# Performance work log

Measured on AMD Instinct MI355X. Metric: run time of the kernel, lower is better.

The kernel has to match this reference:

```python
import math
import jax, jax.numpy as jnp
import numpy as np

# ---- static config (mirrors init_kwargs) ----
NLAT_I, NLON_I = 240, 480      # input equiangular grid (incl. both poles)
NLAT_O, NLON_O = 361, 720      # output equiangular grid (incl. both poles)
CI, CO = 32, 32
NR, NPHI = 3, 3                # kernel_shape
K = (NR - 1) * NPHI + 1        # anisotropic piecewise-linear DISCO basis size = 7
LMAX = 120
CUTOFF = (NR + 0.25) * math.pi / LMAX     # _compute_cutoff_radius
DLAT_O = math.pi / (NLAT_O - 1)
WOFF = int(math.ceil(CUTOFF / DLAT_O))    # half lat-window (=10); geodesic dist >= |dtheta| so window is exact
WLAT = 2 * WOFF + 1
TWO_PI = 2.0 * math.pi


def _bilinear_upsample(x):
    # ResampleS2(mode='bilinear'): x [B,C,NLAT_I,NLON_I] -> [B,C,NLAT_O,NLON_O]
    # equiangular colatitudes theta_j = pi*j/(nlat-1); periodic longitude.
    pos_t = jnp.linspace(0.0, math.pi, NLAT_O) / (math.pi / (NLAT_I - 1))
    i0 = jnp.clip(jnp.floor(pos_t).astype(jnp.int32), 0, NLAT_I - 1)
    i1 = jnp.minimum(i0 + 1, NLAT_I - 1)
    wt = (pos_t - i0).astype(x.dtype)
    xl = (1.0 - wt)[:, None] * x[:, :, i0, :] + wt[:, None] * x[:, :, i1, :]
    pos_p = (jnp.arange(NLON_O) * (TWO_PI / NLON_O)) / (TWO_PI / NLON_I)
    j0f = jnp.floor(pos_p)
    j0 = j0f.astype(jnp.int32) % NLON_I
    j1 = (j0 + 1) % NLON_I
    wp = (pos_p - j0f).astype(x.dtype)
    return (1.0 - wp) * xl[..., j0] + wp * xl[..., j1]


def _build_psi():
    # DISCO filter tensor psi[k, t_out, dlat, dlon] with quadrature merged in,
    # exploiting longitude translation invariance (computed at lon_out = 0).
    theta = jnp.linspace(0.0, math.pi, NLAT_O)
    t_idx = jnp.arange(NLAT_O)
    d_idx = jnp.arange(WLAT) - WOFF
    lat_in = t_idx[:, None] + d_idx[None, :]             # [T,W]
    valid = (lat_in >= 0) & (lat_in < NLAT_O)
    lat_in_c = jnp.clip(lat_in, 0, NLAT_O - 1)
    alpha = -theta[:, None, None]                         # [T,1,1]
    gamma = theta[lat_in_c][:, :, None]                   # [T,W,1]
    beta = (TWO_PI / NLON_O) * jnp.arange(NLON_O)[None, None, :]
    # rotate input point into frame where the output point is at the north pole
    z = jnp.cos(alpha) * jnp.cos(gamma) - jnp.cos(beta) * jnp.sin(alpha) * jnp.sin(gamma)
    xx = jnp.cos(alpha) * jnp.cos(beta) * jnp.sin(gamma) + jnp.sin(alpha) * jnp.cos(gamma)
    yy = jnp.sin(beta) * jnp.sin(gamma)
    r = jnp.arccos(jnp.clip(z, -1.0, 1.0))                # geodesic distance [T,W,P]
    phi = jnp.arctan2(yy, xx) % TWO_PI                    # local azimuth
    dr = CUTOFF / NR
    dph = TWO_PI / NPHI
    vals = [jnp.maximum(0.0, 1.0 - r / dr)]               # isotropic center hat
    for k in range(1, K):
        ir = (k - 1) // NPHI + 1
        ip = (k - 1) % NPHI
        rad = jnp.maximum(0.0, 1.0 - jnp.abs(r - ir * dr) / dr)
        dd = jnp.abs(phi - ip * dph)
        dd = jnp.minimum(dd, TWO_PI - dd)
        az = jnp.maximum(0.0, 1.0 - dd / dph)
        vals.append(rad * az)
    psi = jnp.stack(vals, 0)                              # [K,T,W,P]
    psi = psi * (r <= CUTOFF) * valid[None, :, :, None]
    # merge quadrature weights of the input grid (sin(theta) dtheta dphi)
    q = jnp.sin(theta) * (math.pi / (NLAT_O - 1)) * (TWO_PI / NLON_O)
    psi = psi * q[lat_in_c][None, :, :, None]
    # nodal L1 normalization per basis function and output node
    scale = jnp.sum(psi, axis=(2, 3), keepdims=True)
    psi = psi / jnp.maximum(scale, 1e-8)
    return psi.astype(jnp.float32), lat_in_c


def _disco_conv(xu, weight, psi, lat_in_c):
    # xu [B,Ci,T,P]; weight [Co,Ci,K]; psi [K,T,W,P]
    h = jnp.einsum('oik,bitp->boktp', weight, xu)         # fold channel mixing first
    Hh = jnp.fft.rfft(h, axis=-1)                         # [B,Co,K,T,F]
    Ph = jnp.conj(jnp.fft.rfft(psi, axis=-1))             # [K,T,W,F]
    yh = jnp.zeros(Hh.shape[:2] + (NLAT_O, Hh.shape[-1]), dtype=Hh.dtype)
    for d in range(WLAT):                                 # small fixed halo loop
        Hd = Hh[:, :, :, lat_in_c[:, d], :]               # [B,Co,K,T,F]
        yh = yh + jnp.einsum('boktf,ktf->botf', Hd, Ph[:, :, d, :])
    return jnp.fft.irfft(yh, n=NLON_O, axis=-1)           # circular correlation over lon


def setup_inputs() -> dict:
    key = jax.random.key(0)
    k1, k2 = jax.random.split(key)
    x = jax.random.normal(k1, (1, CI, NLAT_I, NLON_I), dtype=jnp.float32)
    weight = jax.random.normal(k2, (CO, CI, K), dtype=jnp.float32) * 0.05
    return {'x': x, 'weight': weight}


def reference(x, weight):
    psi, lat_in_c = _build_psi()
    xu = _bilinear_upsample(x.astype(jnp.float32))        # forced fp32 region
    y = _disco_conv(xu, weight.astype(jnp.float32), psi, lat_in_c)
    return y.astype(x.dtype)
```

## Files before the change

kernel.cpp:

```cpp
#include <hip/hip_runtime.h>
#include <hip/hip_bf16.h>
#include <math.h>

#define NLAT_I 240
#define NLON_I 480
#define NLAT_O 361
#define NLON_O 720
#define CI_N 32
#define CO_N 32
#define K_N 7
#define WOFF 10
#define WLAT 21

#define PI_F 3.14159265358979323846f
#define TWOPI_F 6.28318530717958647692f
#define DLAT_V (PI_F / 360.0f)
#define DPHI_V (TWOPI_F / 720.0f)
#define CUTOFF_V (3.25f * PI_F / 120.0f)
#define DR_V (CUTOFF_V / 3.0f)
#define IDR_V (1.0f / DR_V)
#define DPH_V (TWOPI_F / 3.0f)
#define IDPH_V (1.0f / DPH_V)
#define QF_V (DLAT_V * DPHI_V)

#define PAD_T 64
#define CT 64
#define NBLK 256
#define NC45 45
#define NE 7581

typedef __attribute__((ext_vector_type(8))) short short8v;
typedef __attribute__((ext_vector_type(4))) short short4v;
typedef __attribute__((ext_vector_type(16))) float f32x16;

__device__ __forceinline__ unsigned short f2bf(float f) {
  __hip_bfloat16 h = __float2bfloat16(f);
  union { __hip_bfloat16 b; unsigned short s; } u; u.b = h; return u.s;
}

__device__ __forceinline__ void psi_eval(float ct, float st, float cg, float sg,
                                         float q, float bang, float v[7]) {
  float sb, cb;
  sincosf(bang, &sb, &cb);
  float dx = sg * cb - st;
  float dy = sg * sb;
  float dz = cg - ct;
  float c2 = dx * dx + dy * dy + dz * dz;
  float r = 2.0f * asinf(fminf(1.0f, 0.5f * sqrtf(c2)));
  if (r <= CUTOFF_V) {
    float xx = ct * cb * sg - st * cg;
    float yy = sb * sg;
    float phi = atan2f(yy, xx);
    if (phi < 0.0f) phi += TWOPI_F;
    v[0] = fmaxf(0.0f, 1.0f - r * IDR_V) * q;
#pragma unroll
    for (int k = 1; k < 7; ++k) {
      const float irdr = (float)(1 + (k - 1) / 3) * DR_V;
      const float ipph = (float)((k - 1) % 3) * DPH_V;
      float rad = fmaxf(0.0f, 1.0f - fabsf(r - irdr) * IDR_V);
      float dd = fabsf(phi - ipph);
      dd = fminf(dd, TWOPI_F - dd);
      float az = fmaxf(0.0f, 1.0f - dd * IDPH_V);
      v[k] = rad * az * q;
    }
  } else {
#pragma unroll
    for (int k = 0; k < 7; ++k) v[k] = 0.0f;
  }
}

__device__ __forceinline__ int windowB(int t, int d) {
  int tp = t + d - WOFF;
  if (tp < 0 || tp > NLAT_O - 1) return -1;
  float th = (float)t * DLAT_V, ga = (float)tp * DLAT_V;
  float st = sinf(th), ct = cosf(th), sg = sinf(ga), cg = cosf(ga);
  float den = st * sg;
  float num = cosf(CUTOFF_V) - ct * cg;
  if (den < 1e-9f) return (fabsf(th - ga) <= CUTOFF_V) ? 360 : -1;
  if (num >= den) return -1;
  if (num <= -den) return 360;
  int B = (int)ceilf(acosf(num / den) * (1.0f / DPHI_V)) + 1;
  return B > 360 ? 360 : B;
}

__device__ __forceinline__ int nsupOf(int B) { return (B >= 360) ? 720 : 2 * B + 1; }
__device__ __forceinline__ int widthOf(int B) {
  return (B < 0) ? 0 : ((nsupOf(B) + 129) & ~1);
}

__global__ void prep_kernel(const float* __restrict__ w, unsigned short* __restrict__ w2,
                            int* __restrict__ offsF, int* __restrict__ offsT,
                            int* __restrict__ wtab, float* __restrict__ sums,
                            int* __restrict__ counter, int* __restrict__ gB,
                            int* __restrict__ gUc) {
  const int tid = threadIdx.x;
  __shared__ int temp[256];
  if (tid < 8) counter[tid] = 0;
  for (int idx = tid; idx < 361 * 7; idx += 256) sums[idx] = 0.0f;
  for (int idx = tid; idx < 14 * 32 * 16; idx += 256) {
    int kk = idx & 15; int o = (idx >> 4) & 31; int c16 = idx >> 9;
    int ci = c16 * 16 + kk; int i = ci & 31; int k = ci >> 5;
    w2[idx] = f2bf(w[(o * 32 + i) * 7 + k]);
  }
  for (int e = tid; e < NE; e += 256) {
    int t = e / 21, d = e % 21;
    int B = windowB(t, d);
    gB[e] = B;
    offsF[e] = (B >= 0) ? nsupOf(B) * 7 : 0;
    offsT[e] = 14 * widthOf(B);
  }
  __syncthreads();
  for (int t = tid; t < 361; t += 256) {
    int run = 0;
    for (int d = 0; d < WLAT; ++d) {
      gUc[t * 22 + d] = run;
      int B = gB[t * 21 + d];
      int np = (B >= 0) ? ((31 + B) >> 4) + ((B + 15) >> 4) + 1 : 0;
      run += np;
    }
    gUc[t * 22 + 21] = run;
    wtab[t] = run;
  }
  __syncthreads();
#pragma unroll 1
  for (int pass = 0; pass < 2; ++pass) {
    int* a = pass ? offsT : offsF;
    int s = tid * 30, e = s + 30; if (e > NE) e = NE; if (s > NE) s = NE;
    int sum = 0;
    for (int i = s; i < e; ++i) sum += a[i];
    temp[tid] = sum;
    __syncthreads();
    if (tid == 0) {
      int run = 0;
      for (int i = 0; i < 256; ++i) { int v = temp[i]; temp[i] = run; run += v; }
      a[NE] = run;
    }
    __syncthreads();
    int run = temp[tid];
    for (int i = s; i < e; ++i) { int v = a[i]; a[i] = run; run += v; }
    __syncthreads();
  }
}

__global__ void upsample_kernel(const float* __restrict__ x,
                                unsigned short* __restrict__ XT) {
  int idx = blockIdx.x * 256 + threadIdx.x;
  if (idx >= NLAT_O * NC45 * 512) return;
  int kk = idx & 15;
  int i = (idx >> 4) & 31;
  int c = (idx >> 9) % NC45;
  int t = idx / (NC45 * 512);
  int p = c * 16 + kk;

  double post = (double)t * (239.0 / 360.0);
  int i0 = (int)floor(post);
  if (i0 < 0) i0 = 0;
  if (i0 > NLAT_I - 1) i0 = NLAT_I - 1;
  int i1 = i0 + 1; if (i1 > NLAT_I - 1) i1 = NLAT_I - 1;
  float wt = (float)(post - (double)i0);

  double posp = (double)p * (2.0 / 3.0);
  double j0f = floor(posp);
  int j0 = ((int)j0f) % NLON_I;
  int j1 = (j0 + 1) % NLON_I;
  float wp = (float)(posp - j0f);

  const float* xi = x + (size_t)i * (NLAT_I * NLON_I);
  float a = xi[i0 * NLON_I + j0];
  float b = xi[i0 * NLON_I + j1];
  float cc = xi[i1 * NLON_I + j0];
  float d = xi[i1 * NLON_I + j1];
  float l0 = (1.0f - wt) * a + wt * cc;
  float l1 = (1.0f - wt) * b + wt * d;
  XT[idx] = f2bf((1.0f - wp) * l0 + wp * l1);
}

__global__ void psi_raw_kernel(const int* __restrict__ offsF,
                               float* __restrict__ PSIF,
                               float* __restrict__ sums) {
  int t = blockIdx.x, d = blockIdx.y;
  int B = windowB(t, d);
  if (B < 0) return;
  int nsup = nsupOf(B);
  int bLo = (B >= 360) ? -360 : -B;
  int offF = offsF[t * 21 + d];
  int tp = t + d - WOFF;
  float th = (float)t * DLAT_V, ga = (float)tp * DLAT_V;
  float st, ct, sg, cg;
  sincosf(th, &st, &ct);
  sincosf(ga, &sg, &cg);
  float q = sg * QF_V;
  float acc[7];
#pragma unroll
  for (int k = 0; k < 7; ++k) acc[k] = 0.0f;
  for (int ix = threadIdx.x; ix < nsup; ix += 256) {
    float v[7];
    psi_eval(ct, st, cg, sg, q, (float)(bLo + ix) * DPHI_V, v);
#pragma unroll
    for (int k = 0; k < 7; ++k) { PSIF[offF + k * nsup + ix] = v[k]; acc[k] += v[k]; }
  }
#pragma unroll
  for (int k = 0; k < 7; ++k) {
    float a = acc[k];
    for (int off = 32; off > 0; off >>= 1) a += __shfl_down(a, off, 64);
    acc[k] = a;
  }
  __shared__ float red[4][7];
  int wid = threadIdx.x >> 6;
  if ((threadIdx.x & 63) == 0) {
#pragma unroll
    for (int k = 0; k < 7; ++k) red[wid][k] = acc[k];
  }
  __syncthreads();
  if (threadIdx.x == 0) {
#pragma unroll
    for (int k = 0; k < 7; ++k)
      atomicAdd(&sums[t * 7 + k], red[0][k] + red[1][k] + red[2][k] + red[3][k]);
  }
}

__global__ void psi_toep_kernel(const int* __restrict__ offsF,
                                const int* __restrict__ offsT,
                                const float* __restrict__ PSIF,
                                const float* __restrict__ sums,
                                unsigned short* __restrict__ PSIT) {
  int t = blockIdx.x, d = blockIdx.y;
  int B = windowB(t, d);
  if (B < 0) return;
  int nsup = nsupOf(B);
  int width = widthOf(B);
  int offF = offsF[t * 21 + d];
  int offT = offsT[t * 21 + d];
  float rc[7];
#pragma unroll
  for (int k = 0; k < 7; ++k) rc[k] = 1.0f / fmaxf(sums[t * 7 + k], 1e-8f);
  for (int ix = threadIdx.x; ix <= width; ix += 256) {
    int isup = ix - PAD_T;
    unsigned short vv[7];
    if (isup >= 0 && isup < nsup) {
#pragma unroll
      for (int k = 0; k < 7; ++k)
        vv[k] = f2bf(PSIF[offF + k * nsup + isup] * rc[k]);
    } else {
#pragma unroll
      for (int k = 0; k < 7; ++k) vv[k] = 0;
    }
    if (ix < width) {
#pragma unroll
      for (int k = 0; k < 7; ++k) PSIT[offT + (2 * k) * width + ix] = vv[k];
    }
    if (ix >= 1) {
#pragma unroll
      for (int k = 0; k < 7; ++k) PSIT[offT + (2 * k + 1) * width + ix - 1] = vv[k];
    }
  }
}


#define LOADSET(S, CC) {                                                  \
    int v45 = pw16 + (CC);                                                \
    if (v45 < 0) v45 += NC45;                                             \
    if (v45 >= NC45) v45 -= NC45;                                         \
    int v45b = v45 + 2; if (v45b >= NC45) v45b -= NC45;                   \
    A##S##a = *(const short8v*)(XT + (((size_t)tpd * NC45 + v45) << 9) + laneA);  \
    A##S##b = *(const short8v*)(XT + (((size_t)tpd * NC45 + v45b) << 9) + laneA); \
    int jbIdx = (CC) * 16 + lconst - bLo + PAD_T;                         \
    const unsigned short* bp = pbase + jbIdx + ((jbIdx & 1) ? (wdt - 1) : 0); \
    B##S##0 = *(const short8v*)(bp);                                      \
    B##S##1 = *(const short8v*)(bp + ks);                                 \
    B##S##2 = *(const short8v*)(bp + 2 * ks);                             \
    B##S##3 = *(const short8v*)(bp + 3 * ks);                             \
    B##S##4 = *(const short8v*)(bp + 4 * ks);                             \
    B##S##5 = *(const short8v*)(bp + 5 * ks);                             \
    B##S##6 = *(const short8v*)(bp + 6 * ks); }

#define MFMASET(S) {                                                      \
    accA0 = __builtin_amdgcn_mfma_f32_32x32x16_bf16(A##S##a, B##S##0, accA0, 0, 0, 0); \
    accB0 = __builtin_amdgcn_mfma_f32_32x32x16_bf16(A##S##b, B##S##0, accB0, 0, 0, 0); \
    accA1 = __builtin_amdgcn_mfma_f32_32x32x16_bf16(A##S##a, B##S##1, accA1, 0, 0, 0); \
    accB1 = __builtin_amdgcn_mfma_f32_32x32x16_bf16(A##S##b, B##S##1, accB1, 0, 0, 0); \
    accA2 = __builtin_amdgcn_mfma_f32_32x32x16_bf16(A##S##a, B##S##2, accA2, 0, 0, 0); \
    accB2 = __builtin_amdgcn_mfma_f32_32x32x16_bf16(A##S##b, B##S##2, accB2, 0, 0, 0); \
    accA3 = __builtin_amdgcn_mfma_f32_32x32x16_bf16(A##S##a, B##S##3, accA3, 0, 0, 0); \
    accB3 = __builtin_amdgcn_mfma_f32_32x32x16_bf16(A##S##b, B##S##3, accB3, 0, 0, 0); \
    accA4 = __builtin_amdgcn_mfma_f32_32x32x16_bf16(A##S##a, B##S##4, accA4, 0, 0, 0); \
    accB4 = __builtin_amdgcn_mfma_f32_32x32x16_bf16(A##S##b, B##S##4, accB4, 0, 0, 0); \
    accA5 = __builtin_amdgcn_mfma_f32_32x32x16_bf16(A##S##a, B##S##5, accA5, 0, 0, 0); \
    accB5 = __builtin_amdgcn_mfma_f32_32x32x16_bf16(A##S##b, B##S##5, accB5, 0, 0, 0); \
    accA6 = __builtin_amdgcn_mfma_f32_32x32x16_bf16(A##S##a, B##S##6, accA6, 0, 0, 0); \
    accB6 = __builtin_amdgcn_mfma_f32_32x32x16_bf16(A##S##b, B##S##6, accB6, 0, 0, 0); }

#define DUMP2(ACC, KK, HB) {                                              \
    short4v q_;                                                           \
    q_[0]=(short)f2bf(ACC[8*(HB)+0]); q_[1]=(short)f2bf(ACC[8*(HB)+1]);   \
    q_[2]=(short)f2bf(ACC[8*(HB)+2]); q_[3]=(short)f2bf(ACC[8*(HB)+3]);   \
    *(short4v*)(b2 + ((KK) << 9) + b0_) = q_;                             \
    q_[0]=(short)f2bf(ACC[8*(HB)+4]); q_[1]=(short)f2bf(ACC[8*(HB)+5]);   \
    q_[2]=(short)f2bf(ACC[8*(HB)+6]); q_[3]=(short)f2bf(ACC[8*(HB)+7]);   \
    *(short4v*)(b2 + ((KK) << 9) + b0_ + 8) = q_; }

#define GEMM2PT(AC0, AC1, AC2, AC3, AC4, AC5, AC6, PTILE) {               \
    f32x16 Dy;                                                            \
    _Pragma("unroll") for (int z = 0; z < 16; ++z) Dy[z] = 0.0f;          \
    DUMP2(AC0, 0, 0) DUMP2(AC1, 1, 0) DUMP2(AC2, 2, 0) DUMP2(AC3, 3, 0)  \
    DUMP2(AC4, 4, 0) DUMP2(AC5, 5, 0) DUMP2(AC6, 6, 0)                    \
    _Pragma("unroll") for (int k2 = 0; k2 < 7; ++k2) {                    \
      short8v A2 = *(const short8v*)(w2g + (((2 * k2 + 0) * 32 + nn) << 4) + g8); \
      short8v B2f = *(const short8v*)(b2 + (k2 << 9) + (nn << 4) + g8);   \
      Dy = __builtin_amdgcn_mfma_f32_32x32x16_bf16(A2, B2f, Dy, 0, 0, 0); \
    }                                                                     \
    DUMP2(AC0, 0, 1) DUMP2(AC1, 1, 1) DUMP2(AC2, 2, 1) DUMP2(AC3, 3, 1)  \
    DUMP2(AC4, 4, 1) DUMP2(AC5, 5, 1) DUMP2(AC6, 6, 1)                    \
    _Pragma("unroll") for (int k2 = 0; k2 < 7; ++k2) {                    \
      short8v A2 = *(const short8v*)(w2g + (((2 * k2 + 1) * 32 + nn) << 4) + g8); \
      short8v B2f = *(const short8v*)(b2 + (k2 << 9) + (nn << 4) + g8);   \
      Dy = __builtin_amdgcn_mfma_f32_32x32x16_bf16(A2, B2f, Dy, 0, 0, 0); \
    }                                                                     \
    const int p_ = (PTILE) * 32 + nn;                                     \
    if (p_ < NLON_O) {                                                    \
      _Pragma("unroll") for (int rr = 0; rr < 16; ++rr) {                 \
        int o = (rr & 3) + 8 * (rr >> 2) + 4 * g;                         \
        atomicAdd(&y[((size_t)o * NLAT_O + t) * NLON_O + p_], Dy[rr]);    \
      }                                                                   \
    } }

__global__ __launch_bounds__(256, 1) void disco_kernel(
    const unsigned short* __restrict__ XT, const unsigned short* __restrict__ PSIT,
    const unsigned short* __restrict__ w2g, const int* __restrict__ offsT,
    const int* __restrict__ wtab, const int* __restrict__ gB,
    const int* __restrict__ gUc, float* __restrict__ y,
    int* __restrict__ counter) {
  const int tid = threadIdx.x;
  __shared__ __align__(16) unsigned short b2all[4 * 3584];
  __shared__ int Sbuf[362];
  __shared__ int sB[WLAT], sUc[WLAT + 1], sOff[WLAT], sW[WLAT];
  __shared__ int curItem, sSv;

  for (int j = tid; j < 361; j += 256) {
    int t = (j & 1) ? 360 - (j >> 1) : (j >> 1);
    Sbuf[j] = 3 * ((wtab[t] + CT - 1) / CT);
  }
  __syncthreads();
  if (tid == 0) {
    int run = 0;
    for (int j = 0; j < 361; ++j) { int v = Sbuf[j]; Sbuf[j] = run; run += v; }
    Sbuf[361] = run;
    sSv = 0;
  }
  __syncthreads();
  const int NTOT = Sbuf[361];
  const int xcd = blockIdx.x & 7;

  const int lane = tid & 63, wv = tid >> 6, nn = lane & 31, g = lane >> 5;
  const int g8 = g * 8;
  const int laneA = nn * 16 + g8;
  const int lconst = g8 - nn;

  while (true) {
    if (tid == 0) {
      int mm = NTOT;
      int s2 = sSv;
      while (s2 < 8) {
        int cx = (xcd + s2) & 7;
        int b0 = (NTOT * cx) >> 3;
        int b1 = (NTOT * (cx + 1)) >> 3;
        int off = atomicAdd(&counter[cx], 1);
        if (b0 + off < b1) { mm = b0 + off; break; }
        ++s2;
      }
      sSv = s2;
      curItem = mm;
    }
    __syncthreads();
    const int m = curItem;
    if (m >= NTOT) break;

    int lo = 0, hi = 360;
    while (lo < hi) {
      int mid = (lo + hi + 1) >> 1;
      if (Sbuf[mid] <= m) lo = mid; else hi = mid - 1;
    }
    const int j = lo;
    const int r = m - Sbuf[j];
    const int t = (j & 1) ? 360 - (j >> 1) : (j >> 1);
    const int pgpair = r % 3;
    const int part = r / 3;

    if (tid < WLAT) {
      int B = gB[t * 21 + tid];
      sB[tid] = B;
      sOff[tid] = offsT[t * 21 + tid];
      sW[tid] = widthOf(B);
    }
    if (tid < WLAT + 1) sUc[tid] = gUc[t * 22 + tid];
    __syncthreads();

    const int Wt = sUc[WLAT];
    int g0 = part * CT, g1 = g0 + CT;
    if (g1 > Wt) g1 = Wt;

    const int ptileA = pgpair * 8 + 2 * wv;
    const int pw16 = ptileA * 2;

    f32x16 accA0, accA1, accA2, accA3, accA4, accA5, accA6;
    f32x16 accB0, accB1, accB2, accB3, accB4, accB5, accB6;
#pragma unroll
    for (int z = 0; z < 16; ++z) {
      accA0[z]=0; accA1[z]=0; accA2[z]=0; accA3[z]=0; accA4[z]=0; accA5[z]=0; accA6[z]=0;
      accB0[z]=0; accB1[z]=0; accB2[z]=0; accB3[z]=0; accB4[z]=0; accB5[z]=0; accB6[z]=0;
    }

    short8v A0a, A0b, A1a, A1b;
    short8v B00, B01, B02, B03, B04, B05, B06;
    short8v B10, B11, B12, B13, B14, B15, B16;

    int gi = g0;
    int d = 0;
    while (d < WLAT && sUc[d + 1] <= gi) ++d;
    while (gi < g1) {
      const int B = sB[d];
      const int bLo = (B >= 360) ? -360 : -B;
      const int cmin = -((B + 15) >> 4);
      const int tpd = t + d - WOFF;
      const int wdt = sW[d];
      const int ks = 2 * wdt;
      const unsigned short* pbase = PSIT + sOff[d];
      const int rend = sUc[d + 1];
      const int gend = (rend < g1) ? rend : g1;
      const int n = gend - gi;
      int c = cmin + (gi - sUc[d]);

      LOADSET(0, c)
      int it = 0;
      for (; it + 2 <= n; it += 2) {
        LOADSET(1, c + 1)
        MFMASET(0)
        if (it + 2 < n) { LOADSET(0, c + 2) }
        MFMASET(1)
        c += 2;
      }
      if (it < n) { MFMASET(0) }

      gi = gend;
      ++d;
      while (d < WLAT && sUc[d + 1] <= gi) ++d;
    }

    unsigned short* b2 = b2all + wv * 3584;
    const int b0_ = nn * 16 + 4 * g;
    GEMM2PT(accA0, accA1, accA2, accA3, accA4, accA5, accA6, ptileA)
    GEMM2PT(accB0, accB1, accB2, accB3, accB4, accB5, accB6, ptileA + 1)
  }
}

extern "C" void kernel_launch(void* const* d_in, const int* in_sizes, int n_in,
                              void* d_out, int out_size, void* d_ws, size_t ws_size,
                              hipStream_t stream) {
  (void)in_sizes; (void)n_in; (void)out_size; (void)ws_size;
  const float* x = (const float*)d_in[0];
  const float* w = (const float*)d_in[1];
  float* y = (float*)d_out;

  unsigned short* XT = (unsigned short*)d_ws;
  float* PSIF = (float*)(XT + (size_t)NLAT_O * NC45 * 512);
  unsigned short* PSIT = (unsigned short*)(PSIF + 6000000);
  unsigned short* w2 = PSIT + 26000000;
  float* sums = (float*)(w2 + 7168);
  int* offsF = (int*)(sums + NLAT_O * K_N);
  int* offsT = offsF + NE + 1;
  int* wtab = offsT + NE + 1;
  int* counter = wtab + 361;
  int* gB = counter + 8;
  int* gUc = gB + NE;

  hipMemsetAsync(y, 0, (size_t)CO_N * NLAT_O * NLON_O * sizeof(float), stream);

  prep_kernel<<<1, 256, 0, stream>>>(w, w2, offsF, offsT, wtab, sums, counter, gB, gUc);
  int n_up = NLAT_O * NC45 * 512;
  upsample_kernel<<<(n_up + 255) / 256, 256, 0, stream>>>(x, XT);
  psi_raw_kernel<<<dim3(NLAT_O, WLAT), 256, 0, stream>>>(offsF, PSIF, sums);
  psi_toep_kernel<<<dim3(NLAT_O, WLAT), 256, 0, stream>>>(offsF, offsT, PSIF, sums, PSIT);
  disco_kernel<<<NBLK, 256, 0, stream>>>(XT, PSIT, w2, offsT, wtab, gB, gUc, y, counter);
}
```

Measured before the change: 532.0 us.

## Stage A/B operand tiles through LDS ring with async global_load_lds pipeline

Replaces the direct per-lane global vector loads of the X and psi operands with a multi-stage LDS ring buffer filled by global_load_lds DMA. The psi rows are shared across the four waves, with each wave fetching part of them. Per-step indexing is precomputed in lane registers and broadcast with readlane, so the inner loop no longer walks the halo structure. The aim is to hide global memory latency and stop each wave from loading psi redundantly, at the cost of a block barrier every step, extra LDS use and reliance on a hand-tuned vmcnt wait.

```diff
diff --git a/kernel.cpp b/kernel.cpp
--- a/kernel.cpp
+++ b/kernel.cpp
@@ -36,6 +36,13 @@
 __device__ __forceinline__ unsigned short f2bf(float f) {
   __hip_bfloat16 h = __float2bfloat16(f);
   union { __hip_bfloat16 b; unsigned short s; } u; u.b = h; return u.s;
+}
+
+typedef __attribute__((address_space(1))) const unsigned int ga_u32_t;
+typedef __attribute__((address_space(3))) unsigned int ls_u32_t;
+__device__ __forceinline__ void dma16(const unsigned short* g, unsigned short* l) {
+  __builtin_amdgcn_global_load_lds((ga_u32_t*)(const void*)g,
+                                   (ls_u32_t*)(void*)l, 16, 0, 0);
 }
 
 __device__ __forceinline__ void psi_eval(float ct, float st, float cg, float sg,
@@ -257,24 +264,47 @@
 }
 
 
-#define LOADSET(S, CC) {                                                  \
-    int v45 = pw16 + (CC);                                                \
-    if (v45 < 0) v45 += NC45;                                             \
-    if (v45 >= NC45) v45 -= NC45;                                         \
-    int v45b = v45 + 2; if (v45b >= NC45) v45b -= NC45;                   \
-    A##S##a = *(const short8v*)(XT + (((size_t)tpd * NC45 + v45) << 9) + laneA);  \
-    A##S##b = *(const short8v*)(XT + (((size_t)tpd * NC45 + v45b) << 9) + laneA); \
-    int jbIdx = (CC) * 16 + lconst - bLo + PAD_T;                         \
-    const unsigned short* bp = pbase + jbIdx + ((jbIdx & 1) ? (wdt - 1) : 0); \
-    B##S##0 = *(const short8v*)(bp);                                      \
-    B##S##1 = *(const short8v*)(bp + ks);                                 \
-    B##S##2 = *(const short8v*)(bp + 2 * ks);                             \
-    B##S##3 = *(const short8v*)(bp + 3 * ks);                             \
-    B##S##4 = *(const short8v*)(bp + 4 * ks);                             \
-    B##S##5 = *(const short8v*)(bp + 5 * ks);                             \
-    B##S##6 = *(const short8v*)(bp + 6 * ks); }
-
-#define MFMASET(S) {                                                      \
+#define VMW16 asm volatile("s_waitcnt vmcnt(16)" ::: "memory");
+#define BARR  __builtin_amdgcn_s_barrier();
+
+#define STAGEU(IDX) {                                                       \
+    int ix_ = (IDX); if (ix_ > nUm1) ix_ = nUm1;                            \
+    int mx_ = __builtin_amdgcn_readlane(mxL, ix_);                          \
+    int my_ = __builtin_amdgcn_readlane(myL, ix_);                          \
+    int wdt_ = my_ & 4095;                                                  \
+    int dd_ = (my_ >> 12) & 31;                                             \
+    int cc_ = ((my_ >> 17) & 63) - 32;                                      \
+    int sl_ = ix_ & 7;                                                      \
+    int jb_ = mx_ + lconst;                                                 \
+    const unsigned short* bs_ = PSIT + jb_ + ((jb_ & 1) ? (wdt_ - 1) : 0);  \
+    unsigned short* bd_ = Bring + sl_ * 3584;                               \
+    int ks_ = 2 * wdt_;                                                     \
+    dma16(bs_ + r0B * ks_, bd_ + (r0B << 9));                               \
+    dma16(bs_ + r1B * ks_, bd_ + (r1B << 9));                               \
+    int v45_ = pw16 + cc_;                                                  \
+    if (v45_ < 0) v45_ += NC45;                                             \
+    if (v45_ >= NC45) v45_ -= NC45;                                         \
+    int v45b_ = v45_ + 2; if (v45b_ >= NC45) v45b_ -= NC45;                 \
+    int tpd_ = t + dd_ - WOFF;                                              \
+    unsigned short* ad_ = Aring + (((wv << 3) + sl_) << 10);                \
+    dma16(XT + (((size_t)(tpd_ * NC45 + v45_)) << 9) + laneA, ad_);         \
+    dma16(XT + (((size_t)(tpd_ * NC45 + v45b_)) << 9) + laneA, ad_ + 512); }
+
+#define READF(S, IDX) {                                                     \
+    int sl_ = (IDX) & 7;                                                    \
+    const unsigned short* bb_ = Bring + sl_ * 3584 + (lane << 3);           \
+    B##S##0 = *(const short8v*)(bb_);                                       \
+    B##S##1 = *(const short8v*)(bb_ + 512);                                 \
+    B##S##2 = *(const short8v*)(bb_ + 1024);                                \
+    B##S##3 = *(const short8v*)(bb_ + 1536);                                \
+    B##S##4 = *(const short8v*)(bb_ + 2048);                                \
+    B##S##5 = *(const short8v*)(bb_ + 2560);                                \
+    B##S##6 = *(const short8v*)(bb_ + 3072);                                \
+    const unsigned short* aa_ = Aring + (((wv << 3) + sl_) << 10) + (lane << 3); \
+    A##S##a = *(const short8v*)(aa_);                                       \
+    A##S##b = *(const short8v*)(aa_ + 512); }
+
+#define MFMA14(S) {                                                         \
     accA0 = __builtin_amdgcn_mfma_f32_32x32x16_bf16(A##S##a, B##S##0, accA0, 0, 0, 0); \
     accB0 = __builtin_amdgcn_mfma_f32_32x32x16_bf16(A##S##b, B##S##0, accB0, 0, 0, 0); \
     accA1 = __builtin_amdgcn_mfma_f32_32x32x16_bf16(A##S##a, B##S##1, accA1, 0, 0, 0); \
@@ -331,6 +361,8 @@
     const int* __restrict__ gUc, float* __restrict__ y,
     int* __restrict__ counter) {
   const int tid = threadIdx.x;
+  __shared__ __align__(16) unsigned short Bring[8 * 3584];
+  __shared__ __align__(16) unsigned short Aring[32 * 1024];
   __shared__ __align__(16) unsigned short b2all[4 * 3584];
   __shared__ int Sbuf[362];
   __shared__ int sB[WLAT], sUc[WLAT + 1], sOff[WLAT], sW[WLAT];
@@ -355,6 +387,8 @@
   const int g8 = g * 8;
   const int laneA = nn * 16 + g8;
   const int lconst = g8 - nn;
+  const int r0B = (wv < 3) ? 2 * wv : 6;
+  const int r1B = (wv < 3) ? 2 * wv + 1 : 6;
 
   while (true) {
     if (tid == 0) {
@@ -398,9 +432,24 @@
     const int Wt = sUc[WLAT];
     int g0 = part * CT, g1 = g0 + CT;
     if (g1 > Wt) g1 = Wt;
+    const int nU = g1 - g0;
+    const int nUm1 = nU - 1;
 
     const int ptileA = pgpair * 8 + 2 * wv;
     const int pw16 = ptileA * 2;
+
+    int mxL, myL;
+    {
+      int uu_ = lane; if (uu_ > nUm1) uu_ = nUm1;
+      int ug_ = g0 + uu_;
+      int dd = 0;
+      while (dd < 20 && sUc[dd + 1] <= ug_) ++dd;
+      int Bv = sB[dd];
+      int bLo_ = (Bv >= 360) ? -360 : -Bv;
+      int cc_ = -((Bv + 15) >> 4) + (ug_ - sUc[dd]);
+      mxL = sOff[dd] + cc_ * 16 - bLo_ + PAD_T;
+      myL = sW[dd] | (dd << 12) | ((cc_ + 32) << 17);
+    }
 
     f32x16 accA0, accA1, accA2, accA3, accA4, accA5, accA6;
     f32x16 accB0, accB1, accB2, accB3, accB4, accB5, accB6;
@@ -410,40 +459,28 @@
       accB0[z]=0; accB1[z]=0; accB2[z]=0; accB3[z]=0; accB4[z]=0; accB5[z]=0; accB6[z]=0;
     }
 
-    short8v A0a, A0b, A1a, A1b;
-    short8v B00, B01, B02, B03, B04, B05, B06;
-    short8v B10, B11, B12, B13, B14, B15, B16;
-
-    int gi = g0;
-    int d = 0;
-    while (d < WLAT && sUc[d + 1] <= gi) ++d;
-    while (gi < g1) {
-      const int B = sB[d];
-      const int bLo = (B >= 360) ? -360 : -B;
-      const int cmin = -((B + 15) >> 4);
-      const int tpd = t + d - WOFF;
-      const int wdt = sW[d];
-      const int ks = 2 * wdt;
-      const unsigned short* pbase = PSIT + sOff[d];
-      const int rend = sUc[d + 1];
-      const int gend = (rend < g1) ? rend : g1;
-      const int n = gend - gi;
-      int c = cmin + (gi - sUc[d]);
-
-      LOADSET(0, c)
-      int it = 0;
-      for (; it + 2 <= n; it += 2) {
-        LOADSET(1, c + 1)
-        MFMASET(0)
-        if (it + 2 < n) { LOADSET(0, c + 2) }
-        MFMASET(1)
-        c += 2;
-      }
-      if (it < n) { MFMASET(0) }
-
-      gi = gend;
-      ++d;
-      while (d < WLAT && sUc[d + 1] <= gi) ++d;
+    short8v AXa, AXb, BX0, BX1, BX2, BX3, BX4, BX5, BX6;
+    short8v AYa, AYb, BY0, BY1, BY2, BY3, BY4, BY5, BY6;
+
+    STAGEU(0) STAGEU(1) STAGEU(2) STAGEU(3) STAGEU(4)
+    VMW16 BARR
+    READF(X, 0)
+
+    int u = 0;
+    while (true) {
+      STAGEU(u + 5)
+      VMW16 BARR
+      int nx = u + 1; bool h1 = (nx < nU); if (!h1) nx = u;
+      READF(Y, nx)
+      MFMA14(X)
+      if (!h1) break;
+      STAGEU(u + 6)
+      VMW16 BARR
+      int nx2 = u + 2; bool h2 = (nx2 < nU); if (!h2) nx2 = nx;
+      READF(X, nx2)
+      MFMA14(Y)
+      if (!h2) break;
+      u += 2;
     }
 
     unsigned short* b2 = b2all + wv * 3584;
```

After: 480.6 us. -9.7%, faster.
